# Optimization experiments

Hardware: AMD Instinct MI355X
Metric: run time of the kernel (lower is better)

The kernel has to match this reference:

```python
import jax, jax.numpy as jnp
import numpy as np

D_MODEL = 1024
NUM_HEAD = 16
D_K = D_MODEL // NUM_HEAD


def setup_inputs() -> dict:
    key = jax.random.key(0)
    ks = jax.random.split(key, 9)
    s = 1.0 / np.sqrt(D_MODEL)
    x = jax.random.normal(ks[0], (2, 2048, D_MODEL), dtype=jnp.float32)
    Wq = jax.random.uniform(ks[1], (D_MODEL, D_MODEL), jnp.float32, -s, s)
    bq = jax.random.uniform(ks[2], (D_MODEL,), jnp.float32, -s, s)
    Wk = jax.random.uniform(ks[3], (D_MODEL, D_MODEL), jnp.float32, -s, s)
    bk = jax.random.uniform(ks[4], (D_MODEL,), jnp.float32, -s, s)
    Wv = jax.random.uniform(ks[5], (D_MODEL, D_MODEL), jnp.float32, -s, s)
    bv = jax.random.uniform(ks[6], (D_MODEL,), jnp.float32, -s, s)
    Wo = jax.random.uniform(ks[7], (D_MODEL, D_MODEL), jnp.float32, -s, s)
    bo = jax.random.uniform(ks[8], (D_MODEL,), jnp.float32, -s, s)
    return {"x": x, "Wq": Wq, "bq": bq, "Wk": Wk, "bk": bk,
            "Wv": Wv, "bv": bv, "Wo": Wo, "bo": bo}


def reference(x, Wq, bq, Wk, bk, Wv, bv, Wo, bo):
    b, n, d = x.shape
    h, dk = NUM_HEAD, D_K
    # Linear projections (torch Linear: x @ W.T + b)
    q = (x @ Wq.T + bq).reshape(b, n, h, dk).transpose(0, 2, 1, 3)  # [b,h,n,dk]
    k = (x @ Wk.T + bk).reshape(b, n, h, dk).transpose(0, 2, 1, 3)
    v = (x @ Wv.T + bv).reshape(b, n, h, dk).transpose(0, 2, 1, 3)
    scores = jnp.einsum('bhqd,bhkd->bhqk', q, k) / jnp.sqrt(jnp.float32(dk))
    attn = jax.nn.softmax(scores, axis=-1)  # [b,h,n,n]
    out = jnp.einsum('bhqk,bhkd->bhqd', attn, v)
    out = out.transpose(0, 2, 1, 3).reshape(b, n, d)
    return out @ Wo.T + bo
```

## Files before the change

kernel.cpp:

```cpp
#include <hip/hip_runtime.h>

#define BATCH   2
#define SEQ     2048
#define DMODEL  1024
#define NHEAD   16
#define DKH     64
#define MTOT    (BATCH*SEQ)
#define KDIM    DMODEL

#define XB    0u
#define WQB   (4u*1024u*1024u)
#define WKB   (5u*1024u*1024u)
#define WVB   (6u*1024u*1024u)
#define WOB   (7u*1024u*1024u)
#define QOFF  (8u*1024u*1024u)
#define KOFF  (12u*1024u*1024u)
#define VOFF  (16u*1024u*1024u)
#define OOFF  (20u*1024u*1024u)

typedef __bf16 bf16x8 __attribute__((ext_vector_type(8)));
typedef __bf16 bf16x4 __attribute__((ext_vector_type(4)));
typedef float  f32x4  __attribute__((ext_vector_type(4)));

__device__ __forceinline__ void async16(const __bf16* g, __bf16* l) {
  __builtin_amdgcn_global_load_lds(
      (const __attribute__((address_space(1))) void*)g,
      (__attribute__((address_space(3))) void*)l, 16, 0, 0);
}

__global__ __launch_bounds__(256) void cvt_fp32_bf16(
    const float* __restrict__ x,  const float* __restrict__ wq,
    const float* __restrict__ wk, const float* __restrict__ wv,
    const float* __restrict__ wo, __bf16* __restrict__ ws)
{
  const float* src; __bf16* dst; int n;
  switch (blockIdx.y) {
    case 0:  src = x;  dst = ws + XB;  n = 4 * 1024 * 1024; break;
    case 1:  src = wq; dst = ws + WQB; n = 1024 * 1024;     break;
    case 2:  src = wk; dst = ws + WKB; n = 1024 * 1024;     break;
    case 3:  src = wv; dst = ws + WVB; n = 1024 * 1024;     break;
    default: src = wo; dst = ws + WOB; n = 1024 * 1024;     break;
  }
  const int i = (blockIdx.x * 256 + threadIdx.x) * 8;
  if (i < n) {
    const float4 a = *(const float4*)(src + i);
    const float4 b = *(const float4*)(src + i + 4);
    bf16x8 o;
    o[0] = (__bf16)a.x; o[1] = (__bf16)a.y; o[2] = (__bf16)a.z; o[3] = (__bf16)a.w;
    o[4] = (__bf16)b.x; o[5] = (__bf16)b.y; o[6] = (__bf16)b.z; o[7] = (__bf16)b.w;
    *(bf16x8*)(dst + i) = o;
  }
}

__device__ __forceinline__ void gemm128_core(
    const __bf16* __restrict__ A, const __bf16* __restrict__ W,
    int m0, int n0, __bf16* A_lds, __bf16* B_lds, f32x4 (&acc)[4][4])
{
  const int t    = threadIdx.x;
  const int w    = t >> 6;
  const int lane = t & 63;
  const int ln15 = lane & 15;
  const int quad = lane >> 4;
  const int wr   = (w >> 1) << 6;
  const int wc   = (w & 1) << 6;

#pragma unroll
  for (int i = 0; i < 4; ++i)
#pragma unroll
    for (int j = 0; j < 4; ++j) acc[i][j] = (f32x4){0.f, 0.f, 0.f, 0.f};

  for (int kt = 0; kt < KDIM; kt += 32) {
    __syncthreads();
#pragma unroll
    for (int issue = 0; issue < 2; ++issue) {
      const int cbase = issue * 256 + (w << 6);
      const int c     = cbase + lane;
      const int row   = c >> 2;
      const int goff  = ((c & 3) ^ (row & 3)) << 3;
      async16(A + (size_t)(m0 + row) * KDIM + kt + goff, A_lds + cbase * 8);
      async16(W + (size_t)(n0 + row) * KDIM + kt + goff, B_lds + cbase * 8);
    }
    __syncthreads();

    bf16x8 af[4], bfr[4];
#pragma unroll
    for (int i = 0; i < 4; ++i) {
      const int row = wr + i * 16 + ln15;
      af[i] = *(const bf16x8*)&A_lds[row * 32 + ((quad ^ (row & 3)) << 3)];
    }
#pragma unroll
    for (int j = 0; j < 4; ++j) {
      const int row = wc + j * 16 + ln15;
      bfr[j] = *(const bf16x8*)&B_lds[row * 32 + ((quad ^ (row & 3)) << 3)];
    }
#pragma unroll
    for (int i = 0; i < 4; ++i)
#pragma unroll
      for (int j = 0; j < 4; ++j)
        acc[i][j] = __builtin_amdgcn_mfma_f32_16x16x32_bf16(af[i], bfr[j], acc[i][j], 0, 0, 0);
  }
}

__global__ __launch_bounds__(256) void qkv_gemm(
    const __bf16* __restrict__ X,
    const __bf16* __restrict__ Wq, const float* __restrict__ bq,
    const __bf16* __restrict__ Wk, const float* __restrict__ bk,
    const __bf16* __restrict__ Wv, const float* __restrict__ bv,
    __bf16* __restrict__ ws)
{
  __shared__ __align__(16) __bf16 A_lds[128 * 32];
  __shared__ __align__(16) __bf16 B_lds[128 * 32];

  const int z = blockIdx.z;
  const __bf16* W    = (z == 0) ? Wq : (z == 1) ? Wk : Wv;
  const float*  bias = (z == 0) ? bq : (z == 1) ? bk : bv;
  __bf16* out = ws + ((z == 0) ? QOFF : (z == 1) ? KOFF : VOFF);
  const float scale = (z == 0) ? 0.125f * 1.44269504088896f : 1.0f;

  const int m0 = blockIdx.x * 128;
  const int n0 = blockIdx.y * 128;

  f32x4 acc[4][4];
  gemm128_core(X, W, m0, n0, A_lds, B_lds, acc);

  const int t = threadIdx.x, w = t >> 6, lane = t & 63;
  const int ln15 = lane & 15, quad = lane >> 4;
  const int wr = (w >> 1) << 6, wc = (w & 1) << 6;

#pragma unroll
  for (int j = 0; j < 4; ++j) {
    const int n  = n0 + wc + j * 16 + ln15;
    const float bj = bias[n];
    const int h = n >> 6, d = n & 63;
#pragma unroll
    for (int i = 0; i < 4; ++i) {
#pragma unroll
      for (int r = 0; r < 4; ++r) {
        const int m = m0 + wr + i * 16 + (quad << 2) + r;
        const int bb = m >> 11, s = m & 2047;
        const float v = (acc[i][j][r] + bj) * scale;
        size_t dst;
        if (z != 2) dst = (((size_t)(bb * NHEAD + h)) * SEQ + s) * DKH + d;
        else        dst = (((size_t)(bb * NHEAD + h)) * DKH + d) * SEQ + s;
        out[dst] = (__bf16)v;
      }
    }
  }
}

__global__ __launch_bounds__(256) void out_gemm(
    const __bf16* __restrict__ A, const __bf16* __restrict__ Wo,
    const float* __restrict__ bo, float* __restrict__ out)
{
  __shared__ __align__(16) __bf16 A_lds[128 * 32];
  __shared__ __align__(16) __bf16 B_lds[128 * 32];

  const int m0 = blockIdx.x * 128;
  const int n0 = blockIdx.y * 128;

  f32x4 acc[4][4];
  gemm128_core(A, Wo, m0, n0, A_lds, B_lds, acc);

  const int t = threadIdx.x, w = t >> 6, lane = t & 63;
  const int ln15 = lane & 15, quad = lane >> 4;
  const int wr = (w >> 1) << 6, wc = (w & 1) << 6;

#pragma unroll
  for (int j = 0; j < 4; ++j) {
    const int n = n0 + wc + j * 16 + ln15;
    const float bj = bo[n];
#pragma unroll
    for (int i = 0; i < 4; ++i) {
#pragma unroll
      for (int r = 0; r < 4; ++r) {
        const int m = m0 + wr + i * 16 + (quad << 2) + r;
        out[(size_t)m * DMODEL + n] = acc[i][j][r] + bj;
      }
    }
  }
}

__global__ __launch_bounds__(256) void attn_kernel(
    const __bf16* __restrict__ Qb, const __bf16* __restrict__ Kb,
    const __bf16* __restrict__ Vtb, __bf16* __restrict__ Ob)
{
  __shared__ __align__(16) __bf16 Qs[64 * 64];
  __shared__ __align__(16) __bf16 Ks[64 * 64];
  __shared__ __align__(16) __bf16 Vs[64 * 64];
  __shared__ __align__(16) __bf16 Ps[4 * 16 * 64];

  const int t = threadIdx.x, w = t >> 6, lane = t & 63;
  const int ln15 = lane & 15, quad = lane >> 4;
  const int b = blockIdx.z, h = blockIdx.y, q0 = blockIdx.x * 64;
  const size_t bh = (size_t)(b * NHEAD + h);

  const __bf16* Qg = Qb + bh * SEQ * DKH + (size_t)q0 * DKH;
  const __bf16* Kg = Kb + bh * SEQ * DKH;
  const __bf16* Vg = Vtb + bh * DKH * SEQ;

#pragma unroll
  for (int issue = 0; issue < 2; ++issue) {
    const int cbase = issue * 256 + (w << 6);
    const int c = cbase + lane;
    const int row = c >> 3;
    const int goff = ((c & 7) ^ (row & 7)) << 3;
    async16(Qg + (size_t)row * DKH + goff, Qs + cbase * 8);
  }
  __syncthreads();

  bf16x8 qa[2];
  {
    const int row = (w << 4) + ln15;
#pragma unroll
    for (int ks = 0; ks < 2; ++ks) {
      const int k = ks * 32 + (quad << 3);
      qa[ks] = *(const bf16x8*)&Qs[row * 64 + ((((k >> 3) ^ (row & 7))) << 3)];
    }
  }

  float l_lane = 0.f;
  f32x4 o[4];
#pragma unroll
  for (int j = 0; j < 4; ++j) o[j] = (f32x4){0.f, 0.f, 0.f, 0.f};

  __bf16* Pw = Ps + (w << 10);

  int pwr[4];
#pragma unroll
  for (int j = 0; j < 4; ++j)
    pwr[j] = ln15 * 64 + (((2 * j + (quad >> 1)) ^ (ln15 & 7)) << 3) + ((quad & 1) << 2);

  for (int kt = 0; kt < SEQ; kt += 64) {
    __syncthreads();
#pragma unroll
    for (int issue = 0; issue < 2; ++issue) {
      const int cbase = issue * 256 + (w << 6);
      const int c = cbase + lane;
      const int row = c >> 3;
      const int goff = ((c & 7) ^ (row & 7)) << 3;
      async16(Kg + (size_t)(kt + row) * DKH + goff, Ks + cbase * 8);
      async16(Vg + (size_t)row * SEQ + kt + goff, Vs + cbase * 8);
    }
    __syncthreads();

    f32x4 s[4];
#pragma unroll
    for (int j = 0; j < 4; ++j) s[j] = (f32x4){0.f, 0.f, 0.f, 0.f};
#pragma unroll
    for (int j = 0; j < 4; ++j) {
      const int row = (j << 4) + ln15;
#pragma unroll
      for (int ks = 0; ks < 2; ++ks) {
        const int k = ks * 32 + (quad << 3);
        bf16x8 kb = *(const bf16x8*)&Ks[row * 64 + ((((k >> 3) ^ (row & 7))) << 3)];
        s[j] = __builtin_amdgcn_mfma_f32_16x16x32_bf16(kb, qa[ks], s[j], 0, 0, 0);
      }
    }

#pragma unroll
    for (int j = 0; j < 4; ++j) {
      bf16x4 pk;
#pragma unroll
      for (int r = 0; r < 4; ++r) {
        const float pv = exp2f(s[j][r]);
        l_lane += pv;
        pk[r] = (__bf16)pv;
      }
      *(bf16x4*)&Pw[pwr[j]] = pk;
    }

#pragma unroll
    for (int kc = 0; kc < 2; ++kc) {
      const int k = kc * 32 + (quad << 3);
      const int prow = ln15;
      bf16x8 pa = *(const bf16x8*)&Pw[prow * 64 + ((((k >> 3) ^ (prow & 7))) << 3)];
#pragma unroll
      for (int j = 0; j < 4; ++j) {
        const int vrow = (j << 4) + ln15;
        bf16x8 vb = *(const bf16x8*)&Vs[vrow * 64 + ((((k >> 3) ^ (vrow & 7))) << 3)];
        o[j] = __builtin_amdgcn_mfma_f32_16x16x32_bf16(pa, vb, o[j], 0, 0, 0);
      }
    }
  }

  l_lane += __shfl_xor(l_lane, 16);
  l_lane += __shfl_xor(l_lane, 32);
  float inv_l[4];
#pragma unroll
  for (int r = 0; r < 4; ++r)
    inv_l[r] = 1.0f / __shfl(l_lane, (quad << 2) + r);

#pragma unroll
  for (int r = 0; r < 4; ++r) {
    const int q = q0 + (w << 4) + (quad << 2) + r;
#pragma unroll
    for (int j = 0; j < 4; ++j) {
      const int d = (j << 4) + ln15;
      Ob[((size_t)(b * SEQ + q)) * DMODEL + h * DKH + d] = (__bf16)(o[j][r] * inv_l[r]);
    }
  }
}

extern "C" void kernel_launch(void* const* d_in, const int* in_sizes, int n_in,
                              void* d_out, int out_size, void* d_ws, size_t ws_size,
                              hipStream_t stream)
{
  const float* x  = (const float*)d_in[0];
  const float* Wq = (const float*)d_in[1];
  const float* bq = (const float*)d_in[2];
  const float* Wk = (const float*)d_in[3];
  const float* bk = (const float*)d_in[4];
  const float* Wv = (const float*)d_in[5];
  const float* bv = (const float*)d_in[6];
  const float* Wo = (const float*)d_in[7];
  const float* bo = (const float*)d_in[8];
  float*  out = (float*)d_out;
  __bf16* ws  = (__bf16*)d_ws;

  cvt_fp32_bf16<<<dim3(2048, 5, 1), 256, 0, stream>>>(x, Wq, Wk, Wv, Wo, ws);

  qkv_gemm<<<dim3(MTOT / 128, DMODEL / 128, 3), 256, 0, stream>>>(
      ws + XB, ws + WQB, bq, ws + WKB, bk, ws + WVB, bv, ws);

  attn_kernel<<<dim3(SEQ / 64, NHEAD, BATCH), 256, 0, stream>>>(
      ws + QOFF, ws + KOFF, ws + VOFF, ws + OOFF);

  out_gemm<<<dim3(MTOT / 128, DMODEL / 128, 1), 256, 0, stream>>>(
      ws + OOFF, ws + WOB, bo, out);
}
```

Baseline: 216.8 us.

## Switch attention to 32x32x16 MFMA with 128-query tiles per block

```diff
diff --git a/kernel.cpp b/kernel.cpp
--- a/kernel.cpp
+++ b/kernel.cpp
@@ -21,6 +21,7 @@
 typedef __bf16 bf16x8 __attribute__((ext_vector_type(8)));
 typedef __bf16 bf16x4 __attribute__((ext_vector_type(4)));
 typedef float  f32x4  __attribute__((ext_vector_type(4)));
+typedef float  f32x16 __attribute__((ext_vector_type(16)));
 
 __device__ __forceinline__ void async16(const __bf16* g, __bf16* l) {
   __builtin_amdgcn_global_load_lds(
@@ -184,14 +185,14 @@
     const __bf16* __restrict__ Qb, const __bf16* __restrict__ Kb,
     const __bf16* __restrict__ Vtb, __bf16* __restrict__ Ob)
 {
-  __shared__ __align__(16) __bf16 Qs[64 * 64];
+  __shared__ __align__(16) __bf16 Qs[128 * 64];
   __shared__ __align__(16) __bf16 Ks[64 * 64];
   __shared__ __align__(16) __bf16 Vs[64 * 64];
-  __shared__ __align__(16) __bf16 Ps[4 * 16 * 64];
+  __shared__ __align__(16) __bf16 Ps[4 * 32 * 72];
 
   const int t = threadIdx.x, w = t >> 6, lane = t & 63;
-  const int ln15 = lane & 15, quad = lane >> 4;
-  const int b = blockIdx.z, h = blockIdx.y, q0 = blockIdx.x * 64;
+  const int ln31 = lane & 31, hl = lane >> 5;
+  const int b = blockIdx.z, h = blockIdx.y, q0 = blockIdx.x * 128;
   const size_t bh = (size_t)(b * NHEAD + h);
 
   const __bf16* Qg = Qb + bh * SEQ * DKH + (size_t)q0 * DKH;
@@ -199,7 +200,7 @@
   const __bf16* Vg = Vtb + bh * DKH * SEQ;
 
 #pragma unroll
-  for (int issue = 0; issue < 2; ++issue) {
+  for (int issue = 0; issue < 4; ++issue) {
     const int cbase = issue * 256 + (w << 6);
     const int c = cbase + lane;
     const int row = c >> 3;
@@ -208,27 +209,20 @@
   }
   __syncthreads();
 
-  bf16x8 qa[2];
-  {
-    const int row = (w << 4) + ln15;
-#pragma unroll
-    for (int ks = 0; ks < 2; ++ks) {
-      const int k = ks * 32 + (quad << 3);
-      qa[ks] = *(const bf16x8*)&Qs[row * 64 + ((((k >> 3) ^ (row & 7))) << 3)];
-    }
+  const int qrow = (w << 5) + ln31;
+  bf16x8 qf[4];
+#pragma unroll
+  for (int ks = 0; ks < 4; ++ks) {
+    const int chunk = ((2 * ks + hl) ^ (qrow & 7));
+    qf[ks] = *(const bf16x8*)&Qs[qrow * 64 + (chunk << 3)];
   }
 
   float l_lane = 0.f;
-  f32x4 o[4];
-#pragma unroll
-  for (int j = 0; j < 4; ++j) o[j] = (f32x4){0.f, 0.f, 0.f, 0.f};
-
-  __bf16* Pw = Ps + (w << 10);
-
-  int pwr[4];
-#pragma unroll
-  for (int j = 0; j < 4; ++j)
-    pwr[j] = ln15 * 64 + (((2 * j + (quad >> 1)) ^ (ln15 & 7)) << 3) + ((quad & 1) << 2);
+  f32x16 o0, o1;
+#pragma unroll
+  for (int r = 0; r < 16; ++r) { o0[r] = 0.f; o1[r] = 0.f; }
+
+  __bf16* Pw = Ps + w * (32 * 72);
 
   for (int kt = 0; kt < SEQ; kt += 64) {
     __syncthreads();
@@ -243,61 +237,62 @@
     }
     __syncthreads();
 
-    f32x4 s[4];
-#pragma unroll
-    for (int j = 0; j < 4; ++j) s[j] = (f32x4){0.f, 0.f, 0.f, 0.f};
-#pragma unroll
-    for (int j = 0; j < 4; ++j) {
-      const int row = (j << 4) + ln15;
-#pragma unroll
-      for (int ks = 0; ks < 2; ++ks) {
-        const int k = ks * 32 + (quad << 3);
-        bf16x8 kb = *(const bf16x8*)&Ks[row * 64 + ((((k >> 3) ^ (row & 7))) << 3)];
-        s[j] = __builtin_amdgcn_mfma_f32_16x16x32_bf16(kb, qa[ks], s[j], 0, 0, 0);
+    f32x16 s0, s1;
+#pragma unroll
+    for (int r = 0; r < 16; ++r) { s0[r] = 0.f; s1[r] = 0.f; }
+#pragma unroll
+    for (int ks = 0; ks < 4; ++ks) {
+      const int r0 = ln31;
+      const int r1 = 32 + ln31;
+      const int c0 = (((2 * ks + hl) ^ (r0 & 7)) << 3);
+      const int c1 = (((2 * ks + hl) ^ (r1 & 7)) << 3);
+      bf16x8 kf0 = *(const bf16x8*)&Ks[r0 * 64 + c0];
+      bf16x8 kf1 = *(const bf16x8*)&Ks[r1 * 64 + c1];
+      s0 = __builtin_amdgcn_mfma_f32_32x32x16_bf16(kf0, qf[ks], s0, 0, 0, 0);
+      s1 = __builtin_amdgcn_mfma_f32_32x32x16_bf16(kf1, qf[ks], s1, 0, 0, 0);
+    }
+
+#pragma unroll
+    for (int kb = 0; kb < 2; ++kb) {
+      const f32x16& s = kb ? s1 : s0;
+#pragma unroll
+      for (int rg = 0; rg < 4; ++rg) {
+        bf16x4 pk;
+#pragma unroll
+        for (int rr = 0; rr < 4; ++rr) {
+          const float pv = exp2f(s[rg * 4 + rr]);
+          l_lane += pv;
+          pk[rr] = (__bf16)pv;
+        }
+        *(bf16x4*)&Pw[ln31 * 72 + kb * 32 + rg * 8 + hl * 4] = pk;
       }
     }
 
 #pragma unroll
-    for (int j = 0; j < 4; ++j) {
-      bf16x4 pk;
-#pragma unroll
-      for (int r = 0; r < 4; ++r) {
-        const float pv = exp2f(s[j][r]);
-        l_lane += pv;
-        pk[r] = (__bf16)pv;
-      }
-      *(bf16x4*)&Pw[pwr[j]] = pk;
-    }
-
-#pragma unroll
-    for (int kc = 0; kc < 2; ++kc) {
-      const int k = kc * 32 + (quad << 3);
-      const int prow = ln15;
-      bf16x8 pa = *(const bf16x8*)&Pw[prow * 64 + ((((k >> 3) ^ (prow & 7))) << 3)];
-#pragma unroll
-      for (int j = 0; j < 4; ++j) {
-        const int vrow = (j << 4) + ln15;
-        bf16x8 vb = *(const bf16x8*)&Vs[vrow * 64 + ((((k >> 3) ^ (vrow & 7))) << 3)];
-        o[j] = __builtin_amdgcn_mfma_f32_16x16x32_bf16(pa, vb, o[j], 0, 0, 0);
-      }
-    }
-  }
-
-  l_lane += __shfl_xor(l_lane, 16);
+    for (int ks = 0; ks < 4; ++ks) {
+      bf16x8 pf = *(const bf16x8*)&Pw[ln31 * 72 + ks * 16 + hl * 8];
+      const int v0 = ln31;
+      const int v1 = 32 + ln31;
+      const int c0 = (((2 * ks + hl) ^ (v0 & 7)) << 3);
+      const int c1 = (((2 * ks + hl) ^ (v1 & 7)) << 3);
+      bf16x8 vf0 = *(const bf16x8*)&Vs[v0 * 64 + c0];
+      bf16x8 vf1 = *(const bf16x8*)&Vs[v1 * 64 + c1];
+      o0 = __builtin_amdgcn_mfma_f32_32x32x16_bf16(pf, vf0, o0, 0, 0, 0);
+      o1 = __builtin_amdgcn_mfma_f32_32x32x16_bf16(pf, vf1, o1, 0, 0, 0);
+    }
+  }
+
   l_lane += __shfl_xor(l_lane, 32);
-  float inv_l[4];
-#pragma unroll
-  for (int r = 0; r < 4; ++r)
-    inv_l[r] = 1.0f / __shfl(l_lane, (quad << 2) + r);
-
-#pragma unroll
-  for (int r = 0; r < 4; ++r) {
-    const int q = q0 + (w << 4) + (quad << 2) + r;
-#pragma unroll
-    for (int j = 0; j < 4; ++j) {
-      const int d = (j << 4) + ln15;
-      Ob[((size_t)(b * SEQ + q)) * DMODEL + h * DKH + d] = (__bf16)(o[j][r] * inv_l[r]);
-    }
+  const float inv = 1.0f / l_lane;
+
+#pragma unroll
+  for (int r = 0; r < 16; ++r) {
+    const int qi = (r & 3) + 8 * (r >> 2) + 4 * hl;
+    const float iq = __shfl(inv, qi);
+    const int q = q0 + (w << 5) + qi;
+    __bf16* rowp = Ob + ((size_t)(b * SEQ + q)) * DMODEL + h * DKH;
+    rowp[ln31]      = (__bf16)(o0[r] * iq);
+    rowp[32 + ln31] = (__bf16)(o1[r] * iq);
   }
 }
 
@@ -322,7 +317,7 @@
   qkv_gemm<<<dim3(MTOT / 128, DMODEL / 128, 3), 256, 0, stream>>>(
       ws + XB, ws + WQB, bq, ws + WKB, bk, ws + WVB, bv, ws);
 
-  attn_kernel<<<dim3(SEQ / 64, NHEAD, BATCH), 256, 0, stream>>>(
+  attn_kernel<<<dim3(SEQ / 128, NHEAD, BATCH), 256, 0, stream>>>(
       ws + QOFF, ws + KOFF, ws + VOFF, ws + OOFF);
 
   out_gemm<<<dim3(MTOT / 128, DMODEL / 128, 1), 256, 0, stream>>>(
```

Result: no change. 215.6 us (-0.5%).
